# Performance work log

Hardware: AMD Instinct MI355X
Metric: run time of the kernel (lower is better)

Reference implementation:

```python
import jax, jax.numpy as jnp
import numpy as np

BS, H, W, C, K = 8, 48, 48, 8, 20
HW = H * W


def setup_inputs() -> dict:
    key = jax.random.key(0)
    k1, k2 = jax.random.split(key)
    # correlation between every source position (dim1 = h*w) and target pixel (h, w)
    correlation_tensor = jax.random.normal(k1, (BS, HW, H, W), dtype=jnp.float32)
    # soft per-class label map already at feature resolution (nearest-resize identity)
    src_lbl_batch_resize = jax.random.uniform(k2, (BS, C, H, W), dtype=jnp.float32)
    return {"correlation_tensor": correlation_tensor,
            "src_lbl_batch_resize": src_lbl_batch_resize}


def reference(correlation_tensor, src_lbl_batch_resize):
    bs, hw, h, w = correlation_tensor.shape
    c = src_lbl_batch_resize.shape[1]
    # top-K source positions per target pixel (torch: argsort dim=1 desc, take K)
    corr_t = jnp.transpose(correlation_tensor, (0, 2, 3, 1))   # (bs, h, w, hw)
    vals, idx = jax.lax.top_k(corr_t, K)                        # (bs, h, w, K)
    lbl_flat = src_lbl_batch_resize.reshape(bs, c, hw)          # (bs, c, hw)
    # gather labels of the K nearest source positions, per batch element
    def gather_lbl(lbl_b, idx_b):
        return lbl_b[:, idx_b]                                  # (c, h, w, K)
    lbl_g = jax.vmap(gather_lbl)(lbl_flat, idx)                 # (bs, c, h, w, K)
    # weighted sum over the K neighbors with their correlation values
    tar_pred = jnp.einsum('bchwk,bhwk->bchw', lbl_g, vals)      # (bs, c, h, w)
    return tar_pred
```

## Files before the change

### kernel.cpp

```cpp
#include <hip/hip_runtime.h>

#define BSZ    8
#define HWDIM  2304
#define NPIX   (BSZ * HWDIM)
#define NCH    8
#define TOPK   20
#define NCHUNK 32
#define CHUNK  72
#define CAPC   13
#define TAU    2.0f
#define QCH    8
#define NQ     4
#define NBATCH 6
#define BLEN   12

__device__ __forceinline__ unsigned int fkey(float v) {
    unsigned int u = __float_as_uint(v);
    return u ^ (unsigned int)(((int)u >> 31) | 0x80000000);
}
__device__ __forceinline__ float fkey_inv(unsigned int k) {
    unsigned int u = (k & 0x80000000u) ? (k ^ 0x80000000u) : ~k;
    return __uint_as_float(u);
}
__device__ __forceinline__ unsigned long long mk64(unsigned int vk, unsigned int s) {
    return ((unsigned long long)vk << 32) | (0xFFFFFFFFu - s);
}

#define PUSH(KEY) do { unsigned long long _k = (KEY); if (_k > d[0]) { d[0] = _k;   \
    _Pragma("unroll") for (int _j = 0; _j < TOPK - 1; ++_j) {                        \
        unsigned long long _a = d[_j], _b = d[_j + 1];                               \
        bool _sw = _a > _b; d[_j] = _sw ? _b : _a; d[_j + 1] = _sw ? _a : _b; } } } while (0)

__global__ __launch_bounds__(256) void k0_transpose(const float* __restrict__ lbl,
                                                    float* __restrict__ lblT) {
    int pix = blockIdx.x * 256 + threadIdx.x;
    int b = pix / HWDIM, p = pix - b * HWDIM;
    const float* src = lbl + (size_t)b * NCH * HWDIM + p;
    float4 lo, hi;
    lo.x = src[0 * HWDIM]; lo.y = src[1 * HWDIM]; lo.z = src[2 * HWDIM]; lo.w = src[3 * HWDIM];
    hi.x = src[4 * HWDIM]; hi.y = src[5 * HWDIM]; hi.z = src[6 * HWDIM]; hi.w = src[7 * HWDIM];
    float4* dst = (float4*)(lblT + (size_t)pix * NCH);
    dst[0] = lo; dst[1] = hi;
}

__global__ __launch_bounds__(256) void k1_filter(const float* __restrict__ corr,
                                                 unsigned char* __restrict__ cntc,
                                                 unsigned int* __restrict__ gval,
                                                 unsigned char* __restrict__ gidx) {
    __shared__ unsigned int  lval[CAPC][512];
    __shared__ unsigned char lidx[CAPC][512];
    const int PIXTILES = NPIX / 512;
    int tile  = blockIdx.x % PIXTILES;
    int chunk = blockIdx.x / PIXTILES;
    int t = threadIdx.x;
    int pix0 = tile * 512 + t * 2;
    int b = pix0 / HWDIM;
    int p0 = pix0 - b * HWDIM;
    int s0 = chunk * CHUNK;
    const float2* ptr = (const float2*)(corr + ((size_t)b * HWDIM + s0) * HWDIM + p0);
    int c0 = 0, c1 = 0;
    for (int batch = 0; batch < NBATCH; ++batch) {
        float2 r[BLEN];
#pragma unroll
        for (int u = 0; u < BLEN; ++u)
            r[u] = ptr[(size_t)(batch * BLEN + u) * (HWDIM / 2)];
#pragma unroll
        for (int u = 0; u < BLEN; ++u) {
            int j = batch * BLEN + u;
            int w0 = c0 < CAPC - 1 ? c0 : CAPC - 1;
            lval[w0][2 * t] = fkey(r[u].x);
            lidx[w0][2 * t] = (unsigned char)j;
            c0 += (r[u].x > TAU) ? 1 : 0;
            int w1 = c1 < CAPC - 1 ? c1 : CAPC - 1;
            lval[w1][2 * t + 1] = fkey(r[u].y);
            lidx[w1][2 * t + 1] = (unsigned char)j;
            c1 += (r[u].y > TAU) ? 1 : 0;
        }
    }
    cntc[(size_t)chunk * NPIX + pix0]     = (unsigned char)c0;
    cntc[(size_t)chunk * NPIX + pix0 + 1] = (unsigned char)c1;
    __syncthreads();
#pragma unroll
    for (int slot = 0; slot < CAPC; ++slot) {
        size_t base = ((size_t)chunk * CAPC + slot) * NPIX + (size_t)tile * 512;
        gval[base + t]        = lval[slot][t];
        gval[base + t + 256]  = lval[slot][t + 256];
        gidx[base + t]        = lidx[slot][t];
        gidx[base + t + 256]  = lidx[slot][t + 256];
    }
}

__global__ __launch_bounds__(256) void k2_fused(const float* __restrict__ corr,
                                                const float* __restrict__ lblT,
                                                const unsigned char* __restrict__ cntc,
                                                const unsigned int* __restrict__ gval,
                                                const unsigned char* __restrict__ gidx,
                                                float* __restrict__ out) {
    __shared__ unsigned long long sd[TOPK][256];
    int t = threadIdx.x;
    int px64 = blockIdx.x * 64;
    {
        int pix = px64 + (t & 63);
        int q = t >> 6;
        int b = pix / HWDIM, p = pix - b * HWDIM;
        unsigned long long d[TOPK];
#pragma unroll
        for (int i = 0; i < TOPK; ++i) d[i] = 0ull;
        for (int cc = 0; cc < QCH; ++cc) {
            int chunk = q * QCH + cc;
            unsigned int nc = cntc[(size_t)chunk * NPIX + pix];
            unsigned int vv[CAPC], ii[CAPC];
#pragma unroll
            for (int s2 = 0; s2 < CAPC; ++s2) {
                size_t base = ((size_t)chunk * CAPC + s2) * NPIX + pix;
                vv[s2] = gval[base];
                ii[s2] = gidx[base];
            }
            bool ov = (nc >= CAPC);
#pragma unroll
            for (int s2 = 0; s2 < CAPC; ++s2)
                if (!ov && s2 < (int)nc)
                    PUSH(mk64(vv[s2], (unsigned)(chunk * CHUNK) + ii[s2]));
            if (__builtin_expect(ov, 0)) {
                const float* cp = corr + ((size_t)b * HWDIM + chunk * CHUNK) * HWDIM + p;
                for (int j2 = 0; j2 < CHUNK; ++j2) {
                    float v = cp[(size_t)j2 * HWDIM];
                    if (v > TAU) PUSH(mk64(fkey(v), (unsigned)(chunk * CHUNK + j2)));
                }
            }
        }
#pragma unroll
        for (int i = 0; i < TOPK; ++i) sd[i][t] = d[i];
    }
    __syncthreads();
    if (t < 64) {
        int pix = px64 + t;
        int b = pix / HWDIM, p = pix - b * HWDIM;
        unsigned long long d[TOPK];
#pragma unroll
        for (int i = 0; i < TOPK; ++i) d[i] = 0ull;
        int ntot = 0;
#pragma unroll
        for (int q = 0; q < NQ; ++q)
#pragma unroll
            for (int i = 0; i < TOPK; ++i) {
                unsigned long long k = sd[i][q * 64 + t];
                if (k != 0ull) { ntot++; PUSH(k); }
            }
        if (__builtin_expect(ntot < TOPK, 0)) {
#pragma unroll
            for (int i = 0; i < TOPK; ++i) d[i] = 0ull;
            const float* cp = corr + (size_t)b * HWDIM * HWDIM + p;
            for (int s = 0; s < HWDIM; ++s)
                PUSH(mk64(fkey(cp[(size_t)s * HWDIM]), (unsigned)s));
        }
        float acc[NCH];
#pragma unroll
        for (int c = 0; c < NCH; ++c) acc[c] = 0.0f;
#pragma unroll
        for (int i = 0; i < TOPK; ++i) {
            float v = fkey_inv((unsigned int)(d[i] >> 32));
            unsigned int s = 0xFFFFFFFFu - (unsigned int)d[i];
            const float4* lp = (const float4*)(lblT + ((size_t)b * HWDIM + s) * NCH);
            float4 lo = lp[0], hi = lp[1];
            acc[0] += v * lo.x; acc[1] += v * lo.y; acc[2] += v * lo.z; acc[3] += v * lo.w;
            acc[4] += v * hi.x; acc[5] += v * hi.y; acc[6] += v * hi.z; acc[7] += v * hi.w;
        }
#pragma unroll
        for (int c = 0; c < NCH; ++c)
            out[((size_t)b * NCH + c) * HWDIM + p] = acc[c];
    }
}

__global__ __launch_bounds__(64) void k_fallback(const float* __restrict__ corr,
                                                 const float* __restrict__ lbl,
                                                 float* __restrict__ out) {
    int pix = blockIdx.x * 64 + threadIdx.x;
    int b = pix / HWDIM, p = pix - b * HWDIM;
    unsigned long long d[TOPK];
#pragma unroll
    for (int i = 0; i < TOPK; ++i) d[i] = 0ull;
    const float* cp = corr + (size_t)b * HWDIM * HWDIM + p;
    for (int s = 0; s < HWDIM; ++s)
        PUSH(mk64(fkey(cp[(size_t)s * HWDIM]), (unsigned)s));
    float acc[NCH];
#pragma unroll
    for (int c = 0; c < NCH; ++c) acc[c] = 0.0f;
    const float* lb = lbl + (size_t)b * NCH * HWDIM;
#pragma unroll
    for (int i = 0; i < TOPK; ++i) {
        float v = fkey_inv((unsigned int)(d[i] >> 32));
        unsigned int s = 0xFFFFFFFFu - (unsigned int)d[i];
#pragma unroll
        for (int c = 0; c < NCH; ++c) acc[c] += v * lb[(size_t)c * HWDIM + s];
    }
#pragma unroll
    for (int c = 0; c < NCH; ++c)
        out[((size_t)b * NCH + c) * HWDIM + p] = acc[c];
}

extern "C" void kernel_launch(void* const* d_in, const int* in_sizes, int n_in,
                              void* d_out, int out_size, void* d_ws, size_t ws_size,
                              hipStream_t stream) {
    const float* corr = (const float*)d_in[0];
    const float* lbl  = (const float*)d_in[1];
    float* out = (float*)d_out;

    auto align256 = [](size_t x) { return (x + 255) & ~(size_t)255; };
    size_t off = 0;
    size_t gval_off = off; off += align256((size_t)NCHUNK * CAPC * NPIX * 4);
    size_t lblT_off = off; off += align256((size_t)NPIX * NCH * 4);
    size_t cntc_off = off; off += align256((size_t)NCHUNK * NPIX);
    size_t gidx_off = off; off += align256((size_t)NCHUNK * CAPC * NPIX);
    size_t needed = off;

    if (ws_size >= needed) {
        unsigned int* gval = (unsigned int*)((char*)d_ws + gval_off);
        float* lblT = (float*)((char*)d_ws + lblT_off);
        unsigned char* cntc = (unsigned char*)((char*)d_ws + cntc_off);
        unsigned char* gidx = (unsigned char*)((char*)d_ws + gidx_off);

        k0_transpose<<<dim3(NPIX / 256), dim3(256), 0, stream>>>(lbl, lblT);
        k1_filter<<<dim3((NPIX / 512) * NCHUNK), dim3(256), 0, stream>>>(corr, cntc, gval, gidx);
        k2_fused<<<dim3(NPIX / 64), dim3(256), 0, stream>>>(corr, lblT, cntc, gval, gidx, out);
    } else {
        k_fallback<<<dim3(NPIX / 64), dim3(64), 0, stream>>>(corr, lbl, out);
    }
}
```

Measured before the change: 343.6 us.

## Select top-K per pixel with a wavefront bitonic sort over pixel-major candidates

The candidate buffers move from chunk-slot-major to pixel-major 16-entry records, written as vector stores from a padded shared-memory layout. The second stage now assigns one 64-lane wavefront per pixel instead of one thread per pixel. Each wavefront prefix-sums the per-chunk counts, compacts up to 128 candidates into shared memory and bitonic-sorts them with cross-lane shuffles. This replaces the serial insertion-sort PUSH chains. The fallback becomes a wave-parallel iterative argmax, and the final weighted sum is spread across 8 lanes. In exchange the candidate cap drops from 13 to 12, the gval/gidx workspace grows by padding each record from 12 to 16 slots, and any pixel with more than 128 candidates takes the slow full-scan path.

```diff
diff --git a/kernel.cpp b/kernel.cpp
--- a/kernel.cpp
+++ b/kernel.cpp
@@ -7,12 +7,13 @@
 #define TOPK   20
 #define NCHUNK 32
 #define CHUNK  72
-#define CAPC   13
+#define CAPC   12
+#define REC    16
 #define TAU    2.0f
-#define QCH    8
-#define NQ     4
 #define NBATCH 6
 #define BLEN   12
+#define LVS    17
+#define LIS    36
 
 __device__ __forceinline__ unsigned int fkey(float v) {
     unsigned int u = __float_as_uint(v);
@@ -47,18 +48,19 @@
                                                  unsigned char* __restrict__ cntc,
                                                  unsigned int* __restrict__ gval,
                                                  unsigned char* __restrict__ gidx) {
-    __shared__ unsigned int  lval[CAPC][512];
-    __shared__ unsigned char lidx[CAPC][512];
+    __shared__ unsigned int  lval[512 * LVS];
+    __shared__ unsigned char lidx[512 * LIS];
     const int PIXTILES = NPIX / 512;
     int tile  = blockIdx.x % PIXTILES;
     int chunk = blockIdx.x / PIXTILES;
     int t = threadIdx.x;
-    int pix0 = tile * 512 + t * 2;
+    int pix0 = tile * 512 + 2 * t;
     int b = pix0 / HWDIM;
     int p0 = pix0 - b * HWDIM;
     int s0 = chunk * CHUNK;
     const float2* ptr = (const float2*)(corr + ((size_t)b * HWDIM + s0) * HWDIM + p0);
     int c0 = 0, c1 = 0;
+    const int r0 = 2 * t, r1 = 2 * t + 1;
     for (int batch = 0; batch < NBATCH; ++batch) {
         float2 r[BLEN];
 #pragma unroll
@@ -68,107 +70,135 @@
         for (int u = 0; u < BLEN; ++u) {
             int j = batch * BLEN + u;
             int w0 = c0 < CAPC - 1 ? c0 : CAPC - 1;
-            lval[w0][2 * t] = fkey(r[u].x);
-            lidx[w0][2 * t] = (unsigned char)j;
+            lval[r0 * LVS + w0] = fkey(r[u].x);
+            lidx[r0 * LIS + w0] = (unsigned char)j;
             c0 += (r[u].x > TAU) ? 1 : 0;
             int w1 = c1 < CAPC - 1 ? c1 : CAPC - 1;
-            lval[w1][2 * t + 1] = fkey(r[u].y);
-            lidx[w1][2 * t + 1] = (unsigned char)j;
+            lval[r1 * LVS + w1] = fkey(r[u].y);
+            lidx[r1 * LIS + w1] = (unsigned char)j;
             c1 += (r[u].y > TAU) ? 1 : 0;
         }
     }
-    cntc[(size_t)chunk * NPIX + pix0]     = (unsigned char)c0;
-    cntc[(size_t)chunk * NPIX + pix0 + 1] = (unsigned char)c1;
-    __syncthreads();
-#pragma unroll
-    for (int slot = 0; slot < CAPC; ++slot) {
-        size_t base = ((size_t)chunk * CAPC + slot) * NPIX + (size_t)tile * 512;
-        gval[base + t]        = lval[slot][t];
-        gval[base + t + 256]  = lval[slot][t + 256];
-        gidx[base + t]        = lidx[slot][t];
-        gidx[base + t + 256]  = lidx[slot][t + 256];
-    }
-}
-
-__global__ __launch_bounds__(256) void k2_fused(const float* __restrict__ corr,
-                                                const float* __restrict__ lblT,
-                                                const unsigned char* __restrict__ cntc,
-                                                const unsigned int* __restrict__ gval,
-                                                const unsigned char* __restrict__ gidx,
-                                                float* __restrict__ out) {
-    __shared__ unsigned long long sd[TOPK][256];
-    int t = threadIdx.x;
-    int px64 = blockIdx.x * 64;
-    {
-        int pix = px64 + (t & 63);
-        int q = t >> 6;
-        int b = pix / HWDIM, p = pix - b * HWDIM;
-        unsigned long long d[TOPK];
-#pragma unroll
-        for (int i = 0; i < TOPK; ++i) d[i] = 0ull;
-        for (int cc = 0; cc < QCH; ++cc) {
-            int chunk = q * QCH + cc;
-            unsigned int nc = cntc[(size_t)chunk * NPIX + pix];
-            unsigned int vv[CAPC], ii[CAPC];
-#pragma unroll
-            for (int s2 = 0; s2 < CAPC; ++s2) {
-                size_t base = ((size_t)chunk * CAPC + s2) * NPIX + pix;
-                vv[s2] = gval[base];
-                ii[s2] = gidx[base];
+#pragma unroll
+    for (int h = 0; h < 2; ++h) {
+        int px = pix0 + h, row = 2 * t + h;
+        uint4 q0, q1, q2, q3;
+        q0.x = lval[row*LVS+ 0]; q0.y = lval[row*LVS+ 1]; q0.z = lval[row*LVS+ 2]; q0.w = lval[row*LVS+ 3];
+        q1.x = lval[row*LVS+ 4]; q1.y = lval[row*LVS+ 5]; q1.z = lval[row*LVS+ 6]; q1.w = lval[row*LVS+ 7];
+        q2.x = lval[row*LVS+ 8]; q2.y = lval[row*LVS+ 9]; q2.z = lval[row*LVS+10]; q2.w = lval[row*LVS+11];
+        q3 = q2;
+        uint4* vr = (uint4*)(gval + (size_t)px * (NCHUNK * REC) + chunk * REC);
+        vr[0] = q0; vr[1] = q1; vr[2] = q2; vr[3] = q3;
+        unsigned int i0 = *(const unsigned int*)&lidx[row * LIS + 0];
+        unsigned int i1 = *(const unsigned int*)&lidx[row * LIS + 4];
+        unsigned int i2 = *(const unsigned int*)&lidx[row * LIS + 8];
+        uint4 qi; qi.x = i0; qi.y = i1; qi.z = i2; qi.w = i2;
+        *(uint4*)(gidx + (size_t)px * (NCHUNK * REC) + chunk * REC) = qi;
+        cntc[(size_t)chunk * NPIX + px] = (unsigned char)(h ? c1 : c0);
+    }
+}
+
+#define STAGE_SHFL(k, j) {                                                    \
+    unsigned long long pA = __shfl_xor(A, (j), 64);                           \
+    unsigned long long pB = __shfl_xor(B, (j), 64);                           \
+    bool up = ((lane & (j)) == 0);                                            \
+    bool dA = ((lane & (k)) == 0);                                            \
+    bool dB = (((lane + 64) & (k)) == 0);                                     \
+    bool gA = (A > pA), gB = (B > pB);                                        \
+    A = ((up == dA) == gA) ? A : pA;                                          \
+    B = ((up == dB) == gB) ? B : pB; }
+
+__global__ __launch_bounds__(256) void k2_select(const float* __restrict__ corr,
+                                                 const float* __restrict__ lblT,
+                                                 const unsigned char* __restrict__ cntc,
+                                                 const unsigned int* __restrict__ gval,
+                                                 const unsigned char* __restrict__ gidx,
+                                                 float* __restrict__ out) {
+    __shared__ unsigned long long kbuf[4][128];
+    __shared__ unsigned int cbuf[4][32];
+    __shared__ unsigned int pbuf[4][32];
+    __shared__ float        svb[4][TOPK];
+    __shared__ unsigned int ssb[4][TOPK];
+    int wid = threadIdx.x >> 6, lane = threadIdx.x & 63;
+    int pix = blockIdx.x * 4 + wid;
+    int b = pix / HWDIM, p = pix - b * HWDIM;
+
+    unsigned int c = (lane < 32) ? (unsigned int)cntc[(size_t)lane * NPIX + pix] : 0u;
+    bool bad = (lane < 32) && (c >= CAPC);
+    unsigned long long badm = __ballot(bad);
+    unsigned int pf = c;
+#pragma unroll
+    for (int d2 = 1; d2 < 32; d2 <<= 1) {
+        unsigned int o = __shfl_up(pf, d2, 64);
+        if (lane >= d2) pf += o;
+    }
+    unsigned int total = __shfl(pf, 31, 64);
+    if (lane < 32) { cbuf[wid][lane] = c; pbuf[wid][lane] = pf - c; }
+    bool fb = (badm != 0ull) || (total < TOPK) || (total > 128);
+
+    if (!fb) {
+        kbuf[wid][lane] = 0ull; kbuf[wid][lane + 64] = 0ull;
+        const unsigned int*  gv = gval + (size_t)pix * (NCHUNK * REC);
+        const unsigned char* gi = gidx + (size_t)pix * (NCHUNK * REC);
+        unsigned int vv[8]; unsigned char jj[8];
+#pragma unroll
+        for (int k = 0; k < 8; ++k) { vv[k] = gv[lane + 64 * k]; jj[k] = gi[lane + 64 * k]; }
+#pragma unroll
+        for (int k = 0; k < 8; ++k) {
+            int e = lane + 64 * k, ch = e >> 4, sl = e & 15;
+            unsigned int cn = cbuf[wid][ch];
+            if ((unsigned int)sl < cn) {
+                int tgt = (int)pbuf[wid][ch] + sl;
+                kbuf[wid][tgt] = mk64(vv[k], (unsigned int)(ch * CHUNK + jj[k]));
             }
-            bool ov = (nc >= CAPC);
-#pragma unroll
-            for (int s2 = 0; s2 < CAPC; ++s2)
-                if (!ov && s2 < (int)nc)
-                    PUSH(mk64(vv[s2], (unsigned)(chunk * CHUNK) + ii[s2]));
-            if (__builtin_expect(ov, 0)) {
-                const float* cp = corr + ((size_t)b * HWDIM + chunk * CHUNK) * HWDIM + p;
-                for (int j2 = 0; j2 < CHUNK; ++j2) {
-                    float v = cp[(size_t)j2 * HWDIM];
-                    if (v > TAU) PUSH(mk64(fkey(v), (unsigned)(chunk * CHUNK + j2)));
-                }
+        }
+        unsigned long long A = kbuf[wid][lane], B = kbuf[wid][lane + 64];
+        STAGE_SHFL(2, 1)
+        STAGE_SHFL(4, 2)  STAGE_SHFL(4, 1)
+        STAGE_SHFL(8, 4)  STAGE_SHFL(8, 2)  STAGE_SHFL(8, 1)
+        STAGE_SHFL(16, 8) STAGE_SHFL(16, 4) STAGE_SHFL(16, 2) STAGE_SHFL(16, 1)
+        STAGE_SHFL(32, 16) STAGE_SHFL(32, 8) STAGE_SHFL(32, 4) STAGE_SHFL(32, 2) STAGE_SHFL(32, 1)
+        STAGE_SHFL(64, 32) STAGE_SHFL(64, 16) STAGE_SHFL(64, 8) STAGE_SHFL(64, 4) STAGE_SHFL(64, 2) STAGE_SHFL(64, 1)
+        { unsigned long long mx = A > B ? A : B, mn = A > B ? B : A; A = mx; B = mn; }
+        STAGE_SHFL(128, 32) STAGE_SHFL(128, 16) STAGE_SHFL(128, 8)
+        STAGE_SHFL(128, 4)  STAGE_SHFL(128, 2)  STAGE_SHFL(128, 1)
+        if (lane < TOPK) {
+            svb[wid][lane] = fkey_inv((unsigned int)(A >> 32));
+            ssb[wid][lane] = 0xFFFFFFFFu - (unsigned int)A;
+        }
+    } else {
+        const float* cp = corr + (size_t)b * HWDIM * HWDIM + p;
+        unsigned int fk[36];
+#pragma unroll
+        for (int i = 0; i < 36; ++i) fk[i] = fkey(cp[(size_t)(i * 64 + lane) * HWDIM]);
+        for (int it = 0; it < TOPK; ++it) {
+            unsigned int m = 0;
+#pragma unroll
+            for (int i = 0; i < 36; ++i) m = m > fk[i] ? m : fk[i];
+#pragma unroll
+            for (int d2 = 1; d2 < 64; d2 <<= 1) { unsigned int o = __shfl_xor(m, d2, 64); m = m > o ? m : o; }
+            int pos = -1;
+#pragma unroll
+            for (int i = 35; i >= 0; --i) if (fk[i] == m) pos = i;
+            unsigned int smy = (pos >= 0) ? (unsigned int)(pos * 64 + lane) : 0xFFFFFFFFu;
+#pragma unroll
+            for (int d2 = 1; d2 < 64; d2 <<= 1) { unsigned int o = __shfl_xor(smy, d2, 64); smy = smy < o ? smy : o; }
+            if (pos >= 0 && (unsigned int)(pos * 64 + lane) == smy) {
+#pragma unroll
+                for (int i = 0; i < 36; ++i) fk[i] = (i == pos) ? 0u : fk[i];
             }
-        }
-#pragma unroll
-        for (int i = 0; i < TOPK; ++i) sd[i][t] = d[i];
-    }
-    __syncthreads();
-    if (t < 64) {
-        int pix = px64 + t;
-        int b = pix / HWDIM, p = pix - b * HWDIM;
-        unsigned long long d[TOPK];
-#pragma unroll
-        for (int i = 0; i < TOPK; ++i) d[i] = 0ull;
-        int ntot = 0;
-#pragma unroll
-        for (int q = 0; q < NQ; ++q)
-#pragma unroll
-            for (int i = 0; i < TOPK; ++i) {
-                unsigned long long k = sd[i][q * 64 + t];
-                if (k != 0ull) { ntot++; PUSH(k); }
-            }
-        if (__builtin_expect(ntot < TOPK, 0)) {
-#pragma unroll
-            for (int i = 0; i < TOPK; ++i) d[i] = 0ull;
-            const float* cp = corr + (size_t)b * HWDIM * HWDIM + p;
-            for (int s = 0; s < HWDIM; ++s)
-                PUSH(mk64(fkey(cp[(size_t)s * HWDIM]), (unsigned)s));
-        }
-        float acc[NCH];
-#pragma unroll
-        for (int c = 0; c < NCH; ++c) acc[c] = 0.0f;
-#pragma unroll
-        for (int i = 0; i < TOPK; ++i) {
-            float v = fkey_inv((unsigned int)(d[i] >> 32));
-            unsigned int s = 0xFFFFFFFFu - (unsigned int)d[i];
-            const float4* lp = (const float4*)(lblT + ((size_t)b * HWDIM + s) * NCH);
-            float4 lo = lp[0], hi = lp[1];
-            acc[0] += v * lo.x; acc[1] += v * lo.y; acc[2] += v * lo.z; acc[3] += v * lo.w;
-            acc[4] += v * hi.x; acc[5] += v * hi.y; acc[6] += v * hi.z; acc[7] += v * hi.w;
-        }
-#pragma unroll
-        for (int c = 0; c < NCH; ++c)
-            out[((size_t)b * NCH + c) * HWDIM + p] = acc[c];
+            if (lane == 0) { svb[wid][it] = fkey_inv(m); ssb[wid][it] = smy; }
+        }
+    }
+    if (lane < NCH) {
+        float sv[TOPK]; unsigned int ss[TOPK];
+#pragma unroll
+        for (int i = 0; i < TOPK; ++i) { sv[i] = svb[wid][i]; ss[i] = ssb[wid][i]; }
+        float acc = 0.f;
+#pragma unroll
+        for (int i = 0; i < TOPK; ++i)
+            acc += sv[i] * lblT[((size_t)b * HWDIM + ss[i]) * NCH + lane];
+        out[((size_t)b * NCH + lane) * HWDIM + p] = acc;
     }
 }
 
@@ -182,7 +212,7 @@
     for (int i = 0; i < TOPK; ++i) d[i] = 0ull;
     const float* cp = corr + (size_t)b * HWDIM * HWDIM + p;
     for (int s = 0; s < HWDIM; ++s)
-        PUSH(mk64(fkey(cp[(size_t)s * HWDIM]), (unsigned)s));
+        PUSH(mk64(fkey(cp[(size_t)s * HWDIM]), (unsigned int)s));
     float acc[NCH];
 #pragma unroll
     for (int c = 0; c < NCH; ++c) acc[c] = 0.0f;
@@ -208,21 +238,21 @@
 
     auto align256 = [](size_t x) { return (x + 255) & ~(size_t)255; };
     size_t off = 0;
-    size_t gval_off = off; off += align256((size_t)NCHUNK * CAPC * NPIX * 4);
+    size_t gval_off = off; off += align256((size_t)NPIX * NCHUNK * REC * 4);
+    size_t gidx_off = off; off += align256((size_t)NPIX * NCHUNK * REC);
+    size_t cntc_off = off; off += align256((size_t)NCHUNK * NPIX);
     size_t lblT_off = off; off += align256((size_t)NPIX * NCH * 4);
-    size_t cntc_off = off; off += align256((size_t)NCHUNK * NPIX);
-    size_t gidx_off = off; off += align256((size_t)NCHUNK * CAPC * NPIX);
     size_t needed = off;
 
     if (ws_size >= needed) {
         unsigned int* gval = (unsigned int*)((char*)d_ws + gval_off);
+        unsigned char* gidx = (unsigned char*)((char*)d_ws + gidx_off);
+        unsigned char* cntc = (unsigned char*)((char*)d_ws + cntc_off);
         float* lblT = (float*)((char*)d_ws + lblT_off);
-        unsigned char* cntc = (unsigned char*)((char*)d_ws + cntc_off);
-        unsigned char* gidx = (unsigned char*)((char*)d_ws + gidx_off);
 
         k0_transpose<<<dim3(NPIX / 256), dim3(256), 0, stream>>>(lbl, lblT);
         k1_filter<<<dim3((NPIX / 512) * NCHUNK), dim3(256), 0, stream>>>(corr, cntc, gval, gidx);
-        k2_fused<<<dim3(NPIX / 64), dim3(256), 0, stream>>>(corr, lblT, cntc, gval, gidx, out);
+        k2_select<<<dim3(NPIX / 4), dim3(256), 0, stream>>>(corr, lblT, cntc, gval, gidx, out);
     } else {
         k_fallback<<<dim3(NPIX / 64), dim3(64), 0, stream>>>(corr, lbl, out);
     }
```

After: 300.9 us. 1.14x faster.
